# Kernel tuning notes

Measured on AMD Instinct MI355X. Metric: run time of the kernel, lower is better.

## Reference

```python
import jax, jax.numpy as jnp
import numpy as np

# Static config (mirrors cfg.MODEL.LOSSES.Center.*)
ALPHA = 0.5
BETA = 0.1
MARGIN = 50.0
SCALE = 1.0
HARD_MINING = False
B, D, C = 512, 512, 100000


def setup_inputs() -> dict:
    key = jax.random.key(0)
    k1, k2, k3 = jax.random.split(key, 3)
    features = jax.random.normal(k1, (B, D), dtype=jnp.float32)
    labels = jax.random.randint(k2, (B,), 0, C, dtype=jnp.int32)
    centers = jax.random.normal(k3, (C, D), dtype=jnp.float32)
    return {"features": features, "labels": labels, "centers": centers}


def softmax_weights(dist, mask):
    # dist: (B, B) (negative distances), mask: (B, B) in {0, 1}
    min_v = jnp.min(dist * mask, axis=1, keepdims=True)
    numerator = jnp.exp(dist - min_v) * mask  # mask also zeroes out masked entries
    Z = jnp.sum(numerator, axis=1, keepdims=True) + 1e-6
    return numerator / Z


def reference(features, labels, centers):
    labels = labels.astype(jnp.int32)
    # gather, detached (torch: self.centers[labels].detach())
    cg = jax.lax.stop_gradient(centers[labels])  # (B, D)
    delta1 = cg - features  # (B, D)

    center_diff = cg[:, None, :] - cg[None, :, :]  # (B, B, D)
    mask = (labels[None, :] != labels[:, None]).astype(jnp.float32)  # (B, B)
    center_dist = jnp.sqrt(jnp.sum(jnp.square(center_diff), axis=2))  # (B, B)
    mask = mask * (center_dist <= MARGIN).astype(jnp.float32)

    W = softmax_weights(-center_dist, mask)  # (B, B)
    delta2 = jnp.sum(center_diff * W[:, :, None], axis=1)  # (B, D)
    # torch: if mask.sum() < 1: delta2 = zeros
    delta2 = jnp.where(jnp.sum(mask) < 1.0, jnp.zeros_like(delta2), delta2)

    new_vals = cg - ALPHA * delta1 - BETA * delta2  # (B, D)
    new_centers = centers.at[labels].set(jax.lax.stop_gradient(new_vals))

    dist = jnp.clip(jnp.square(cg - features), 1e-12, 1e12)
    loss = jnp.mean(dist) * SCALE
    return loss, new_centers
```

## Files before the change

kernel.cpp:

```cpp
#include <hip/hip_runtime.h>

#define B 512
#define D 512
#define NC 100000
#define BETA 0.1f
#define MARGIN 50.0f
#define TPB 256
#define NFLOAT (NC * D)
#define NG 12800000
#define KAE 4350001
#define KBE 8700001

typedef float f4 __attribute__((ext_vector_type(4)));

__device__ __forceinline__ void copy_span(const f4* __restrict__ src4, f4* __restrict__ dst4,
                                          int lo, int hi, int bi, int nblk, int tid)
{
    const int total = hi - lo;
    const int per = (total + nblk - 1) / nblk;
    const int s = lo + bi * per;
    int e = s + per; if (e > hi) e = hi;
    if (s >= hi) return;
    const int lane = tid & 63;
    int base = s;
    for (; base + 8 * TPB <= e; base += 8 * TPB) {
        const int g = base + tid;
        f4 v[8];
        #pragma unroll
        for (int u = 0; u < 8; ++u) v[u] = src4[g + u * TPB];
        float pw[8];
        #pragma unroll
        for (int u = 0; u < 8; ++u) {
            pw[u] = __shfl_up(v[u].w, 1, 64);
            if (lane == 0) pw[u] = src4[g + u * TPB - 1].w;
        }
        #pragma unroll
        for (int u = 0; u < 8; ++u) {
            f4 o = { pw[u], v[u].x, v[u].y, v[u].z };
            __builtin_nontemporal_store(o, dst4 + (g + u * TPB));
        }
    }
    for (; base < e; base += TPB) {
        const int g = base + tid;
        const int gc = (g < hi) ? g : (hi - 1);
        f4 v = src4[gc];
        float pw = __shfl_up(v.w, 1, 64);
        if (lane == 0) pw = src4[gc - 1].w;
        if (g < e) {
            f4 o = { pw, v.x, v.y, v.z };
            __builtin_nontemporal_store(o, dst4 + g);
        }
    }
}

__global__ __launch_bounds__(TPB) void kA_gather(
    const float* __restrict__ centers, const float* __restrict__ features,
    const int* __restrict__ labels, float* __restrict__ cgbuf,
    float* __restrict__ rowLoss, int* __restrict__ winner, int* __restrict__ maskCnt,
    float* __restrict__ outAll)
{
    const int b = blockIdx.x, t = threadIdx.x;
    if (b < B) {
        __shared__ float red[TPB];
        __shared__ int labs[B];
        __shared__ int wsh;
        if (b == 0 && t == 0) *maskCnt = 0;
        labs[t] = labels[t]; labs[t + 256] = labels[t + 256];
        if (t == 0) wsh = 1;
        __syncthreads();
        const int i = b;
        const int li = labs[i];
        const float2* crow = (const float2*)(centers + (size_t)li * D);
        const float2* frow = (const float2*)(features + (size_t)i * D);
        float2 c = crow[t], f = frow[t];
        ((float2*)(cgbuf + (size_t)i * D))[t] = c;
        float dx = c.x - f.x, dy = c.y - f.y;
        red[t] = fminf(fmaxf(dx * dx, 1e-12f), 1e12f) + fminf(fmaxf(dy * dy, 1e-12f), 1e12f);
        for (int j = i + 1 + t; j < B; j += TPB)
            if (labs[j] == li) wsh = 0;
        __syncthreads();
        for (int s = 128; s; s >>= 1) { if (t < s) red[t] += red[t + s]; __syncthreads(); }
        if (t == 0) { rowLoss[i] = red[0]; winner[i] = wsh; }
    } else {
        copy_span((const f4*)centers, (f4*)outAll, 1, KAE, b - 512, 1536, t);
    }
}

__global__ __launch_bounds__(TPB) void kB_pairdist(
    const float* __restrict__ centers, const int* __restrict__ labels,
    const float* __restrict__ cgbuf, float* __restrict__ dist,
    int* __restrict__ maskCnt, float* __restrict__ outAll)
{
    const int b = blockIdx.x, t = threadIdx.x;
    if (b < 256) {
        __shared__ float As[16][33];
        __shared__ float Bs[16][33];
        __shared__ int redI[TPB];
        const int bi = b >> 4, bj = b & 15;
        const int tx = t & 15, ty = t >> 4;
        float a00 = 0.f, a01 = 0.f, a10 = 0.f, a11 = 0.f;
        for (int k0 = 0; k0 < D; k0 += 16) {
            #pragma unroll
            for (int it = 0; it < 2; ++it) {
                int idx = t + it * 256;
                int r = idx >> 4, kk = idx & 15;
                As[kk][r] = cgbuf[(size_t)(bi * 32 + r) * D + k0 + kk];
                Bs[kk][r] = cgbuf[(size_t)(bj * 32 + r) * D + k0 + kk];
            }
            __syncthreads();
            #pragma unroll
            for (int kk = 0; kk < 16; ++kk) {
                float x0 = As[kk][ty * 2], x1 = As[kk][ty * 2 + 1];
                float y0 = Bs[kk][tx * 2], y1 = Bs[kk][tx * 2 + 1];
                float d00 = x0 - y0, d01 = x0 - y1, d10 = x1 - y0, d11 = x1 - y1;
                a00 += d00 * d00; a01 += d01 * d01; a10 += d10 * d10; a11 += d11 * d11;
            }
            __syncthreads();
        }
        const int r0 = bi * 32 + ty * 2, c0 = bj * 32 + tx * 2;
        float s00 = sqrtf(a00), s01 = sqrtf(a01), s10 = sqrtf(a10), s11 = sqrtf(a11);
        dist[r0 * B + c0]           = s00;
        dist[r0 * B + c0 + 1]       = s01;
        dist[(r0 + 1) * B + c0]     = s10;
        dist[(r0 + 1) * B + c0 + 1] = s11;
        const int lr0 = labels[r0], lr1 = labels[r0 + 1];
        const int lc0 = labels[c0], lc1 = labels[c0 + 1];
        int cnt = 0;
        cnt += (lr0 != lc0) && (s00 <= MARGIN);
        cnt += (lr0 != lc1) && (s01 <= MARGIN);
        cnt += (lr1 != lc0) && (s10 <= MARGIN);
        cnt += (lr1 != lc1) && (s11 <= MARGIN);
        redI[t] = cnt; __syncthreads();
        for (int s = 128; s; s >>= 1) { if (t < s) redI[t] += redI[t + s]; __syncthreads(); }
        if (t == 0 && redI[0] > 0) atomicAdd(maskCnt, redI[0]);
    } else {
        copy_span((const f4*)centers, (f4*)outAll, KAE, KBE, b - 256, 1792, t);
    }
}

__global__ __launch_bounds__(TPB) void kC_gemm(
    const float* __restrict__ features, const int* __restrict__ labels,
    const float* __restrict__ centers, const float* __restrict__ cgbuf,
    const float* __restrict__ dist, const int* __restrict__ maskCnt,
    const float* __restrict__ rowLoss, float* __restrict__ vals,
    float* __restrict__ out, float* __restrict__ outAll)
{
    const int b = blockIdx.x, t = threadIdx.x;
    float* outC = out + 1;
    if (b < 256) {
        __shared__ float As[16][33];
        __shared__ float Bs[16][33];
        __shared__ int labs[B];
        __shared__ float mxs[32], invZs[32], rowSsh[32];
        labs[t] = labels[t]; labs[t + 256] = labels[t + 256];
        __syncthreads();
        const int bi = b >> 4, bj = b & 15;
        {
            const int rg = t >> 3, lg = t & 7;
            const int row = bi * 32 + rg;
            const int lr = labs[row];
            const float* drow = dist + row * B;
            float mx = 0.f;
            for (int k = 0; k < 64; ++k) {
                int j = lg + 8 * k;
                float d = drow[j];
                bool m = (labs[j] != lr) && (d <= MARGIN);
                mx = fmaxf(mx, m ? d : 0.f);
            }
            #pragma unroll
            for (int o = 1; o < 8; o <<= 1) mx = fmaxf(mx, __shfl_xor(mx, o, 64));
            float sum = 0.f;
            for (int k = 0; k < 64; ++k) {
                int j = lg + 8 * k;
                float d = drow[j];
                bool m = (labs[j] != lr) && (d <= MARGIN);
                sum += m ? expf(mx - d) : 0.f;
            }
            #pragma unroll
            for (int o = 1; o < 8; o <<= 1) sum += __shfl_xor(sum, o, 64);
            if (lg == 0) {
                float Z = sum + 1e-6f;
                mxs[rg] = mx; invZs[rg] = 1.f / Z; rowSsh[rg] = sum / Z;
            }
        }
        __syncthreads();
        const float flagv = (*maskCnt > 0) ? 1.f : 0.f;
        const int tx = t & 15, ty = t >> 4;
        float a00 = 0.f, a01 = 0.f, a10 = 0.f, a11 = 0.f;
        for (int j0 = 0; j0 < B; j0 += 16) {
            #pragma unroll
            for (int it = 0; it < 2; ++it) {
                int idx = t + it * 256;
                int r = idx >> 4, jj = idx & 15;
                int j = j0 + jj;
                float d = dist[(size_t)(bi * 32 + r) * B + j];
                bool m = (labs[j] != labs[bi * 32 + r]) && (d <= MARGIN);
                As[jj][r] = m ? expf(mxs[r] - d) * invZs[r] : 0.f;
                int c = idx & 31, jj2 = idx >> 5;
                Bs[jj2][c] = cgbuf[(size_t)(j0 + jj2) * D + bj * 32 + c];
            }
            __syncthreads();
            #pragma unroll
            for (int kk = 0; kk < 16; ++kk) {
                float w0 = As[kk][ty * 2], w1 = As[kk][ty * 2 + 1];
                float c0 = Bs[kk][tx * 2], c1 = Bs[kk][tx * 2 + 1];
                a00 += w0 * c0; a01 += w0 * c1; a10 += w1 * c0; a11 += w1 * c1;
            }
            __syncthreads();
        }
        const int i0 = bi * 32 + ty * 2, i1 = i0 + 1;
        const int dcol = bj * 32 + tx * 2;
        const float s0 = rowSsh[ty * 2], s1 = rowSsh[ty * 2 + 1];
        float c, f;
        c = cgbuf[(size_t)i0 * D + dcol];     f = features[(size_t)i0 * D + dcol];
        vals[(size_t)i0 * D + dcol]     = 0.5f * (c + f) - BETA * flagv * (s0 * c - a00);
        c = cgbuf[(size_t)i0 * D + dcol + 1]; f = features[(size_t)i0 * D + dcol + 1];
        vals[(size_t)i0 * D + dcol + 1] = 0.5f * (c + f) - BETA * flagv * (s0 * c - a01);
        c = cgbuf[(size_t)i1 * D + dcol];     f = features[(size_t)i1 * D + dcol];
        vals[(size_t)i1 * D + dcol]     = 0.5f * (c + f) - BETA * flagv * (s1 * c - a10);
        c = cgbuf[(size_t)i1 * D + dcol + 1]; f = features[(size_t)i1 * D + dcol + 1];
        vals[(size_t)i1 * D + dcol + 1] = 0.5f * (c + f) - BETA * flagv * (s1 * c - a11);
    } else if (b == 256) {
        __shared__ float red[TPB];
        red[t] = rowLoss[t] + rowLoss[t + 256]; __syncthreads();
        for (int s = 128; s; s >>= 1) { if (t < s) red[t] += red[t + s]; __syncthreads(); }
        if (t == 0) out[0] = red[0] * (1.0f / ((float)B * (float)D));
        if (t == 1) { outC[0] = centers[0]; outC[1] = centers[1]; outC[2] = centers[2]; }
        if (t == 2) { outC[NFLOAT - 1] = centers[NFLOAT - 1]; }
    } else {
        copy_span((const f4*)centers, (f4*)outAll, KBE, NG, b - 257, 1791, t);
    }
}

__global__ __launch_bounds__(TPB) void kD_scatter(
    const float* __restrict__ vals, const int* __restrict__ labels,
    const int* __restrict__ winner, float* __restrict__ outC)
{
    const int b = blockIdx.x, t = threadIdx.x;
    const int i = b * 2 + (t >> 7);
    const int dcol = (t & 127) * 4;
    if (!winner[i]) return;
    f4 v;
    __builtin_memcpy(&v, &vals[(size_t)i * D + dcol], 16);
    float* dst = outC + (size_t)labels[i] * D + dcol;
    __builtin_memcpy(dst, &v, 16);
}

extern "C" void kernel_launch(void* const* d_in, const int* in_sizes, int n_in,
                              void* d_out, int out_size, void* d_ws, size_t ws_size,
                              hipStream_t stream)
{
    const float* features = (const float*)d_in[0];
    const int*   labels   = (const int*)d_in[1];
    const float* centers  = (const float*)d_in[2];

    float* out  = (float*)d_out;
    float* outC = out + 1;

    char* ws = (char*)d_ws;
    float* cgbuf   = (float*)(ws);
    float* dist    = (float*)(ws + 1048576);
    float* vals    = (float*)(ws + 2097152);
    float* rowLoss = (float*)(ws + 3145728);
    int*   winner  = (int*)  (ws + 3147776);
    int*   maskCnt = (int*)  (ws + 3149824);

    kA_gather<<<2048, TPB, 0, stream>>>(centers, features, labels, cgbuf, rowLoss,
                                        winner, maskCnt, out);
    kB_pairdist<<<2048, TPB, 0, stream>>>(centers, labels, cgbuf, dist, maskCnt, out);
    kC_gemm<<<2048, TPB, 0, stream>>>(features, labels, centers, cgbuf, dist, maskCnt,
                                      rowLoss, vals, out, out);
    kD_scatter<<<256, TPB, 0, stream>>>(vals, labels, winner, outC);
}
```

Baseline: 124.2 us.

## Merge gather and pair-distance kernels, rebalance background center copy

Folds the gather/loss kernel into the pairwise-distance kernel. The distance tiles now read center rows directly through labels instead of waiting for a gathered buffer, which removes one launch and one dependency stage. The bulk copy of the centers into the output is split across two kernels instead of three, with a new split point and a grid-stride wave-group copy loop. The maskCnt reset moves to a hipMemsetAsync. This adds a memset call and does indirect label-based loads inside the distance tiles.

```diff
diff --git a/kernel.cpp b/kernel.cpp
--- a/kernel.cpp
+++ b/kernel.cpp
@@ -8,94 +8,57 @@
 #define TPB 256
 #define NFLOAT (NC * D)
 #define NG 12800000
-#define KAE 4350001
-#define KBE 8700001
+#define CSPLIT 5335268
 
 typedef float f4 __attribute__((ext_vector_type(4)));
 
-__device__ __forceinline__ void copy_span(const f4* __restrict__ src4, f4* __restrict__ dst4,
-                                          int lo, int hi, int bi, int nblk, int tid)
-{
-    const int total = hi - lo;
-    const int per = (total + nblk - 1) / nblk;
-    const int s = lo + bi * per;
-    int e = s + per; if (e > hi) e = hi;
-    if (s >= hi) return;
-    const int lane = tid & 63;
-    int base = s;
-    for (; base + 8 * TPB <= e; base += 8 * TPB) {
-        const int g = base + tid;
+__device__ __forceinline__ void copy_groups(const f4* __restrict__ src4, f4* __restrict__ dst4,
+                                            int lo, int hi, int widx, int wstride)
+{
+    const int lane = widx & 63;
+    int g = lo + widx;
+    for (; (g - lane) + 63 + 7 * wstride < hi; g += 8 * wstride) {
         f4 v[8];
         #pragma unroll
-        for (int u = 0; u < 8; ++u) v[u] = src4[g + u * TPB];
+        for (int u = 0; u < 8; ++u) v[u] = src4[g + u * wstride];
         float pw[8];
         #pragma unroll
         for (int u = 0; u < 8; ++u) {
             pw[u] = __shfl_up(v[u].w, 1, 64);
-            if (lane == 0) pw[u] = src4[g + u * TPB - 1].w;
+            if (lane == 0) pw[u] = src4[g + u * wstride - 1].w;
         }
         #pragma unroll
         for (int u = 0; u < 8; ++u) {
             f4 o = { pw[u], v[u].x, v[u].y, v[u].z };
-            __builtin_nontemporal_store(o, dst4 + (g + u * TPB));
-        }
-    }
-    for (; base < e; base += TPB) {
-        const int g = base + tid;
-        const int gc = (g < hi) ? g : (hi - 1);
+            __builtin_nontemporal_store(o, dst4 + (g + u * wstride));
+        }
+    }
+    for (; (g - lane) < hi; g += wstride) {
+        int gc = (g < hi) ? g : (hi - 1);
         f4 v = src4[gc];
         float pw = __shfl_up(v.w, 1, 64);
         if (lane == 0) pw = src4[gc - 1].w;
-        if (g < e) {
+        if (g < hi) {
             f4 o = { pw, v.x, v.y, v.z };
             __builtin_nontemporal_store(o, dst4 + g);
         }
     }
 }
 
-__global__ __launch_bounds__(TPB) void kA_gather(
+__global__ __launch_bounds__(TPB) void k1_dist(
     const float* __restrict__ centers, const float* __restrict__ features,
-    const int* __restrict__ labels, float* __restrict__ cgbuf,
+    const int* __restrict__ labels, float* __restrict__ cgbuf, float* __restrict__ dist,
     float* __restrict__ rowLoss, int* __restrict__ winner, int* __restrict__ maskCnt,
     float* __restrict__ outAll)
-{
-    const int b = blockIdx.x, t = threadIdx.x;
-    if (b < B) {
-        __shared__ float red[TPB];
-        __shared__ int labs[B];
-        __shared__ int wsh;
-        if (b == 0 && t == 0) *maskCnt = 0;
-        labs[t] = labels[t]; labs[t + 256] = labels[t + 256];
-        if (t == 0) wsh = 1;
-        __syncthreads();
-        const int i = b;
-        const int li = labs[i];
-        const float2* crow = (const float2*)(centers + (size_t)li * D);
-        const float2* frow = (const float2*)(features + (size_t)i * D);
-        float2 c = crow[t], f = frow[t];
-        ((float2*)(cgbuf + (size_t)i * D))[t] = c;
-        float dx = c.x - f.x, dy = c.y - f.y;
-        red[t] = fminf(fmaxf(dx * dx, 1e-12f), 1e12f) + fminf(fmaxf(dy * dy, 1e-12f), 1e12f);
-        for (int j = i + 1 + t; j < B; j += TPB)
-            if (labs[j] == li) wsh = 0;
-        __syncthreads();
-        for (int s = 128; s; s >>= 1) { if (t < s) red[t] += red[t + s]; __syncthreads(); }
-        if (t == 0) { rowLoss[i] = red[0]; winner[i] = wsh; }
-    } else {
-        copy_span((const f4*)centers, (f4*)outAll, 1, KAE, b - 512, 1536, t);
-    }
-}
-
-__global__ __launch_bounds__(TPB) void kB_pairdist(
-    const float* __restrict__ centers, const int* __restrict__ labels,
-    const float* __restrict__ cgbuf, float* __restrict__ dist,
-    int* __restrict__ maskCnt, float* __restrict__ outAll)
 {
     const int b = blockIdx.x, t = threadIdx.x;
     if (b < 256) {
         __shared__ float As[16][33];
         __shared__ float Bs[16][33];
+        __shared__ int labs[B];
         __shared__ int redI[TPB];
+        labs[t] = labels[t]; labs[t + 256] = labels[t + 256];
+        __syncthreads();
         const int bi = b >> 4, bj = b & 15;
         const int tx = t & 15, ty = t >> 4;
         float a00 = 0.f, a01 = 0.f, a10 = 0.f, a11 = 0.f;
@@ -104,8 +67,8 @@
             for (int it = 0; it < 2; ++it) {
                 int idx = t + it * 256;
                 int r = idx >> 4, kk = idx & 15;
-                As[kk][r] = cgbuf[(size_t)(bi * 32 + r) * D + k0 + kk];
-                Bs[kk][r] = cgbuf[(size_t)(bj * 32 + r) * D + k0 + kk];
+                As[kk][r] = centers[(size_t)labs[bi * 32 + r] * D + k0 + kk];
+                Bs[kk][r] = centers[(size_t)labs[bj * 32 + r] * D + k0 + kk];
             }
             __syncthreads();
             #pragma unroll
@@ -123,8 +86,8 @@
         dist[r0 * B + c0 + 1]       = s01;
         dist[(r0 + 1) * B + c0]     = s10;
         dist[(r0 + 1) * B + c0 + 1] = s11;
-        const int lr0 = labels[r0], lr1 = labels[r0 + 1];
-        const int lc0 = labels[c0], lc1 = labels[c0 + 1];
+        const int lr0 = labs[r0], lr1 = labs[r0 + 1];
+        const int lc0 = labs[c0], lc1 = labs[c0 + 1];
         int cnt = 0;
         cnt += (lr0 != lc0) && (s00 <= MARGIN);
         cnt += (lr0 != lc1) && (s01 <= MARGIN);
@@ -133,12 +96,32 @@
         redI[t] = cnt; __syncthreads();
         for (int s = 128; s; s >>= 1) { if (t < s) redI[t] += redI[t + s]; __syncthreads(); }
         if (t == 0 && redI[0] > 0) atomicAdd(maskCnt, redI[0]);
+    } else if (b < 768) {
+        __shared__ float red[TPB];
+        __shared__ int labs2[B];
+        __shared__ int wsh;
+        labs2[t] = labels[t]; labs2[t + 256] = labels[t + 256];
+        if (t == 0) wsh = 1;
+        __syncthreads();
+        const int i = b - 256;
+        const int li = labs2[i];
+        const float2* crow = (const float2*)(centers + (size_t)li * D);
+        const float2* frow = (const float2*)(features + (size_t)i * D);
+        float2 c = crow[t], f = frow[t];
+        ((float2*)(cgbuf + (size_t)i * D))[t] = c;
+        float dx = c.x - f.x, dy = c.y - f.y;
+        red[t] = fminf(fmaxf(dx * dx, 1e-12f), 1e12f) + fminf(fmaxf(dy * dy, 1e-12f), 1e12f);
+        for (int j = i + 1 + t; j < B; j += TPB)
+            if (labs2[j] == li) wsh = 0;
+        __syncthreads();
+        for (int s = 128; s; s >>= 1) { if (t < s) red[t] += red[t + s]; __syncthreads(); }
+        if (t == 0) { rowLoss[i] = red[0]; winner[i] = wsh; }
     } else {
-        copy_span((const f4*)centers, (f4*)outAll, KAE, KBE, b - 256, 1792, t);
-    }
-}
-
-__global__ __launch_bounds__(TPB) void kC_gemm(
+        copy_groups((const f4*)centers, (f4*)outAll, 1, CSPLIT, (b - 768) * TPB + t, 1280 * TPB);
+    }
+}
+
+__global__ __launch_bounds__(TPB) void k2_gemm(
     const float* __restrict__ features, const int* __restrict__ labels,
     const float* __restrict__ centers, const float* __restrict__ cgbuf,
     const float* __restrict__ dist, const int* __restrict__ maskCnt,
@@ -228,11 +211,11 @@
         if (t == 1) { outC[0] = centers[0]; outC[1] = centers[1]; outC[2] = centers[2]; }
         if (t == 2) { outC[NFLOAT - 1] = centers[NFLOAT - 1]; }
     } else {
-        copy_span((const f4*)centers, (f4*)outAll, KBE, NG, b - 257, 1791, t);
-    }
-}
-
-__global__ __launch_bounds__(TPB) void kD_scatter(
+        copy_groups((const f4*)centers, (f4*)outAll, CSPLIT, NG, (b - 257) * TPB + t, 1791 * TPB);
+    }
+}
+
+__global__ __launch_bounds__(TPB) void k3_scatter(
     const float* __restrict__ vals, const int* __restrict__ labels,
     const int* __restrict__ winner, float* __restrict__ outC)
 {
@@ -265,10 +248,10 @@
     int*   winner  = (int*)  (ws + 3147776);
     int*   maskCnt = (int*)  (ws + 3149824);
 
-    kA_gather<<<2048, TPB, 0, stream>>>(centers, features, labels, cgbuf, rowLoss,
-                                        winner, maskCnt, out);
-    kB_pairdist<<<2048, TPB, 0, stream>>>(centers, labels, cgbuf, dist, maskCnt, out);
-    kC_gemm<<<2048, TPB, 0, stream>>>(features, labels, centers, cgbuf, dist, maskCnt,
+    hipMemsetAsync(maskCnt, 0, sizeof(int), stream);
+    k1_dist<<<2048, TPB, 0, stream>>>(centers, features, labels, cgbuf, dist,
+                                      rowLoss, winner, maskCnt, out);
+    k2_gemm<<<2048, TPB, 0, stream>>>(features, labels, centers, cgbuf, dist, maskCnt,
                                       rowLoss, vals, out, out);
-    kD_scatter<<<256, TPB, 0, stream>>>(vals, labels, winner, outC);
-}
+    k3_scatter<<<256, TPB, 0, stream>>>(vals, labels, winner, outC);
+}
```

New measurement: 118.0 us. -5.0%, faster.
